# Kernel tuning notes

Measured on AMD Instinct MI355X. Metric: run time of the kernel, lower is better.

Reference implementation:

```python
import jax, jax.numpy as jnp
import numpy as np

B, S, E, H, STEPS = 32, 2048, 300, 256, 24


def setup_inputs() -> dict:
    key = jax.random.key(0)
    ks = jax.random.split(key, 16)
    sc = 0.05
    inp = {
        "input_ids": jax.random.normal(ks[0], (B, S, E), dtype=jnp.float32),
        "tree_ids": jax.random.randint(ks[1], (B, STEPS, S), 0, S),
        "tree_ids_r": jax.random.randint(ks[2], (B, STEPS, S), 0, S),
        "tree_ids_l": jax.random.randint(ks[3], (B, STEPS, S), 0, S),
        # N-ary (binary) TreeLSTM parameters (Tai et al. 2015)
        "W_iou": jax.random.normal(ks[4], (E, 3 * H), dtype=jnp.float32) * sc,
        "b_iou": jnp.zeros((3 * H,), dtype=jnp.float32),
        "U_iou_l": jax.random.normal(ks[5], (H, 3 * H), dtype=jnp.float32) * sc,
        "U_iou_r": jax.random.normal(ks[6], (H, 3 * H), dtype=jnp.float32) * sc,
        "W_f": jax.random.normal(ks[7], (E, H), dtype=jnp.float32) * sc,
        "b_f": jnp.zeros((H,), dtype=jnp.float32),
        "U_f_ll": jax.random.normal(ks[8], (H, H), dtype=jnp.float32) * sc,
        "U_f_lr": jax.random.normal(ks[9], (H, H), dtype=jnp.float32) * sc,
        "U_f_rl": jax.random.normal(ks[10], (H, H), dtype=jnp.float32) * sc,
        "U_f_rr": jax.random.normal(ks[11], (H, H), dtype=jnp.float32) * sc,
    }
    return inp


def _gather_nodes(t, idx):
    # t: [B,S,H], idx: [B,S] -> [B,S,H]
    return jnp.take_along_axis(t, idx[..., None], axis=1)


def reference(input_ids, tree_ids, tree_ids_r, tree_ids_l,
              W_iou, b_iou, U_iou_l, U_iou_r,
              W_f, b_f, U_f_ll, U_f_lr, U_f_rl, U_f_rr):
    dt = input_ids.dtype
    h0 = jnp.zeros((B, S, H), dtype=dt)
    c0 = jnp.zeros((B, S, H), dtype=dt)
    # input projections are step-invariant: compute once
    x_iou = input_ids @ W_iou + b_iou          # [B,S,3H]
    x_f = input_ids @ W_f + b_f                # [B,S,H]
    bidx = jnp.arange(B)[:, None]              # [B,1]

    def step(carry, ids):
        h, c = carry
        idd, idl, idr = ids                    # each [B,S]
        h_l = _gather_nodes(h, idl); c_l = _gather_nodes(c, idl)
        h_r = _gather_nodes(h, idr); c_r = _gather_nodes(c, idr)
        iou = x_iou + h_l @ U_iou_l + h_r @ U_iou_r
        i, o, u = jnp.split(iou, 3, axis=-1)
        i = jax.nn.sigmoid(i); o = jax.nn.sigmoid(o); u = jnp.tanh(u)
        f_l = jax.nn.sigmoid(x_f + h_l @ U_f_ll + h_r @ U_f_lr)
        f_r = jax.nn.sigmoid(x_f + h_l @ U_f_rl + h_r @ U_f_rr)
        c_new = i * u + f_l * c_l + f_r * c_r
        h_new = o * jnp.tanh(c_new)
        # scatter updates to destination node ids; slot 0 is the null slot
        h = h.at[bidx, idd].set(h_new)
        c = c.at[bidx, idd].set(c_new)
        h = h.at[:, 0].set(0.0)
        c = c.at[:, 0].set(0.0)
        return (h, c), None

    ids_seq = (jnp.transpose(tree_ids, (1, 0, 2)),
               jnp.transpose(tree_ids_l, (1, 0, 2)),
               jnp.transpose(tree_ids_r, (1, 0, 2)))
    (h, c), _ = jax.lax.scan(step, (h0, c0), ids_seq)

    roots = tree_ids[:, -1, :].max(axis=1)     # [B]
    h_root = jnp.take_along_axis(
        h, jnp.broadcast_to(roots[:, None, None], (B, 1, H)), axis=1)[:, 0]
    return (h, c, h_root)
```

## Files before the change

kernel.cpp:

```cpp
#include <hip/hip_runtime.h>
#include <hip/hip_bf16.h>
#include <math.h>

#define B_     32
#define S_     2048
#define E_     300
#define H_     256
#define STEPS_ 24
#define BS_    (B_ * S_)
#define NPACK  1280
#define KSL    16
#define KSLP   10
#define COPYB  1024

typedef __bf16 bf16x8 __attribute__((ext_vector_type(8)));
typedef float  f32x4  __attribute__((ext_vector_type(4)));

__device__ __forceinline__ float sigm(float x) {
    return 1.0f / (1.0f + __expf(-x));
}
__device__ __forceinline__ float fast_tanh(float x) {
    return 2.0f * sigm(2.0f * x) - 1.0f;
}

__global__ __launch_bounds__(256) void pack_B_kernel(
    const float* __restrict__ U_iou_l, const float* __restrict__ U_iou_r,
    const float* __restrict__ U_f_ll,  const float* __restrict__ U_f_lr,
    const float* __restrict__ U_f_rl,  const float* __restrict__ U_f_rr,
    __hip_bfloat16* __restrict__ Bp)
{
    const int idx = blockIdx.x * 256 + threadIdx.x;
    if (idx >= KSL * NPACK * 32) return;
    const int ks = idx / (NPACK * 32);
    const int rem = idx - ks * (NPACK * 32);
    const int p = rem >> 5;
    const int kin = rem & 31;
    const int k = ks * 32 + kin;
    const int w = p / 80;
    const int rg = p - w * 80;
    const int g = rg >> 4;
    const int c = w * 16 + (rg & 15);
    float v;
    if (g < 3) {
        const int col = g * 256 + c;
        v = (k < 256) ? U_iou_l[k * 768 + col] : U_iou_r[(k - 256) * 768 + col];
    } else if (g == 3) {
        v = (k < 256) ? U_f_ll[k * 256 + c] : U_f_lr[(k - 256) * 256 + c];
    } else {
        v = (k < 256) ? U_f_rl[k * 256 + c] : U_f_rr[(k - 256) * 256 + c];
    }
    Bp[idx] = __float2bfloat16(v);
}

__global__ __launch_bounds__(256) void pack_W_kernel(
    const float* __restrict__ W_iou, const float* __restrict__ W_f,
    __hip_bfloat16* __restrict__ Wp)
{
    const int idx = blockIdx.x * 256 + threadIdx.x;
    if (idx >= KSLP * 1024 * 32) return;
    const int ks = idx / (1024 * 32);
    const int rem = idx - ks * (1024 * 32);
    const int p = rem >> 5;
    const int kin = rem & 31;
    const int k = ks * 32 + kin;
    const int cw = p >> 6;
    const int g = (p >> 4) & 3;
    const int col = cw * 16 + (p & 15);
    float v = 0.f;
    if (k < E_) v = (g < 3) ? W_iou[k * 768 + g * 256 + col] : W_f[k * 256 + col];
    Wp[idx] = __float2bfloat16(v);
}

__global__ __launch_bounds__(256) void winner_kernel(
    const int* __restrict__ tree_ids, int* __restrict__ winner)
{
    const int idx = blockIdx.x * 256 + threadIdx.x;
    if (idx >= B_ * STEPS_ * S_) return;
    const int b = idx / (STEPS_ * S_);
    const int rem = idx - b * (STEPS_ * S_);
    const int t = rem / S_;
    const int s = rem - t * S_;
    const int d = tree_ids[idx];
    if ((unsigned)d < (unsigned)S_)
        atomicMax(&winner[(size_t)t * BS_ + b * S_ + d], s);
}

__global__ __launch_bounds__(256) void compact_kernel(
    const int* __restrict__ winner, int* __restrict__ compact,
    int* __restrict__ count)
{
    const int tb = blockIdx.x;
    const int tid = threadIdx.x;
    const int* w = winner + (size_t)tb * S_;
    int* cmp = compact + (size_t)tb * S_;
    __shared__ int scan_[256];
    __shared__ int base_;
    if (tid == 0) base_ = 0;
    __syncthreads();
    for (int chunk = 0; chunk < S_ / 256; ++chunk) {
        const int d = chunk * 256 + tid;
        const int s = w[d];
        const int p = (d != 0 && s >= 0) ? 1 : 0;
        int v = p;
        scan_[tid] = v;
        __syncthreads();
        for (int off = 1; off < 256; off <<= 1) {
            const int add = (tid >= off) ? scan_[tid - off] : 0;
            __syncthreads();
            v += add;
            scan_[tid] = v;
            __syncthreads();
        }
        const int mybase = base_;
        if (p) cmp[mybase + v - 1] = (s << 11) | d;
        __syncthreads();
        if (tid == 0) base_ += scan_[255];
        __syncthreads();
    }
    if (tid == 0) count[tb] = base_;
}

__global__ __launch_bounds__(256) void proj_kernel(
    const float* __restrict__ input, const __hip_bfloat16* __restrict__ Wp,
    const float* __restrict__ b_iou, const float* __restrict__ b_f,
    __hip_bfloat16* __restrict__ x_pack)
{
    __shared__ __hip_bfloat16 Ash[16][328];
    const int tid = threadIdx.x;
    const int row0 = blockIdx.x * 16;

    for (int it = 0; it < 5; ++it) {
        const int idx = tid + it * 256;
        const int r = idx / 80;
        const int c4 = idx - r * 80;
        float4 v = make_float4(0.f, 0.f, 0.f, 0.f);
        if (c4 < 75) v = *(const float4*)(input + (size_t)(row0 + r) * E_ + c4 * 4);
        union { __hip_bfloat16 h[4]; uint2 u; } tconv;
        tconv.h[0] = __float2bfloat16(v.x);
        tconv.h[1] = __float2bfloat16(v.y);
        tconv.h[2] = __float2bfloat16(v.z);
        tconv.h[3] = __float2bfloat16(v.w);
        *(uint2*)&Ash[r][c4 * 4] = tconv.u;
    }
    __syncthreads();

    const int lane = tid & 63;
    const int wave = tid >> 6;
    const int m16 = lane & 15;
    const int q = lane >> 4;

    f32x4 acc[16];
    const f32x4 z4 = {0.f, 0.f, 0.f, 0.f};
#pragma unroll
    for (int nt = 0; nt < 16; ++nt) acc[nt] = z4;

    const __hip_bfloat16* wp = Wp + ((size_t)(wave * 256 + m16)) * 32 + q * 8;
    for (int ks = 0; ks < KSLP; ++ks) {
        const bf16x8 a = *reinterpret_cast<const bf16x8*>(&Ash[m16][ks * 32 + q * 8]);
        const __hip_bfloat16* wk = wp + (size_t)ks * 32768;
#pragma unroll
        for (int nt = 0; nt < 16; ++nt) {
            const bf16x8 bb = *reinterpret_cast<const bf16x8*>(wk + nt * 512);
            acc[nt] = __builtin_amdgcn_mfma_f32_16x16x32_bf16(a, bb, acc[nt], 0, 0, 0);
        }
    }

#pragma unroll
    for (int j = 0; j < 4; ++j) {
        const int row = row0 + q * 4 + j;
        const size_t xrow = (size_t)row * 1024;
#pragma unroll
        for (int chunk = 0; chunk < 4; ++chunk) {
            const int c = (wave * 4 + chunk) * 16 + m16;
            union { __hip_bfloat16 h[4]; uint2 u; } pk;
            pk.h[0] = __float2bfloat16(acc[chunk * 4 + 0][j] + b_iou[c]);
            pk.h[1] = __float2bfloat16(acc[chunk * 4 + 1][j] + b_iou[256 + c]);
            pk.h[2] = __float2bfloat16(acc[chunk * 4 + 2][j] + b_iou[512 + c]);
            pk.h[3] = __float2bfloat16(acc[chunk * 4 + 3][j] + b_f[c]);
            *(uint2*)(x_pack + xrow + (size_t)c * 4) = pk.u;
        }
    }
}

__global__ __launch_bounds__(256, 4) void step_kernel(
    const __hip_bfloat16* __restrict__ h_cur, const __hip_bfloat16* __restrict__ c_cur,
    __hip_bfloat16* __restrict__ h_next, __hip_bfloat16* __restrict__ c_next,
    const int* __restrict__ tree_ids_l, const int* __restrict__ tree_ids_r,
    const int* __restrict__ winner_t, const int* __restrict__ compact,
    const int* __restrict__ count, const __hip_bfloat16* __restrict__ x_pack,
    const __hip_bfloat16* __restrict__ Bp, int t)
{
    const int tid = threadIdx.x;

    if (blockIdx.x < COPYB) {
        const uint4* h_cur4 = (const uint4*)h_cur;
        const uint4* c_cur4 = (const uint4*)c_cur;
        uint4* h_next4 = (uint4*)h_next;
        uint4* c_next4 = (uint4*)c_next;
#pragma unroll
        for (int i = 0; i < 8; ++i) {
            const int idx = blockIdx.x * 256 + tid + i * (COPYB * 256);
            const int row = idx >> 5;
            const int d = row & (S_ - 1);
            if (d == 0) {
                const uint4 z = make_uint4(0u, 0u, 0u, 0u);
                h_next4[idx] = z;
                c_next4[idx] = z;
            } else if (winner_t[row] < 0) {
                h_next4[idx] = h_cur4[idx];
                c_next4[idx] = c_cur4[idx];
            }
        }
        return;
    }

    const int sb     = blockIdx.x - COPYB;
    const int grp    = sb >> 5;
    const int l32    = sb & 31;
    const int nq     = l32 >> 3;
    const int tile_g = grp * 8 + (l32 & 7);
    const int b    = tile_g >> 6;
    const int tile = tile_g & 63;
    const int nAct = count[t * B_ + b];
    const int s0 = tile * 32;
    if (s0 >= nAct) return;

    __shared__ __hip_bfloat16 Ash[32][520];
    __shared__ int sS[32], sD[32], sIdl[32], sIdr[32];

    const int* cmp = compact + ((size_t)(t * B_ + b)) * S_;
    if (tid < 32) {
        const int gi = s0 + tid;
        const int pair = (gi < nAct) ? cmp[gi] : 0;
        sS[tid] = pair >> 11;
        sD[tid] = pair & 2047;
    }
    __syncthreads();

    const int* idl_b = tree_ids_l + ((size_t)b * STEPS_ + t) * S_;
    const int* idr_b = tree_ids_r + ((size_t)b * STEPS_ + t) * S_;
    if (tid < 32)       sIdl[tid]      = idl_b[sS[tid]];
    else if (tid < 64)  sIdr[tid - 32] = idr_b[sS[tid - 32]];
    __syncthreads();

#pragma unroll
    for (int it = 0; it < 8; ++it) {
        const int idx = tid + it * 256;
        const int r = idx >> 6;
        const int ch = idx & 63;
        const int half = ch >> 5;
        const int c16 = ch & 31;
        const int src = half ? sIdr[r] : sIdl[r];
        const uint4 v = *(const uint4*)(h_cur + ((size_t)(b * S_) + src) * H_ + c16 * 8);
        *(uint4*)&Ash[r][half * 256 + c16 * 8] = v;
    }
    __syncthreads();

    const int lane = tid & 63;
    const int wave = tid >> 6;
    const int m16 = lane & 15;
    const int q = lane >> 4;
    const int w16 = nq * 4 + wave;
    const int cg = w16 * 16 + m16;

    f32x4 acc[2][5];
#pragma unroll
    for (int sm = 0; sm < 2; ++sm) {
#pragma unroll
        for (int j = 0; j < 4; ++j) {
            const int r = sm * 16 + q * 4 + j;
            float xi = 0.f, xo = 0.f, xu = 0.f, xf = 0.f;
            if (sD[r] != 0) {
                const size_t xrow = ((size_t)(b * S_ + sS[r])) * 1024;
                union { uint2 u; __hip_bfloat16 x[4]; } xv;
                xv.u = *(const uint2*)(x_pack + xrow + (size_t)cg * 4);
                xi = __bfloat162float(xv.x[0]);
                xo = __bfloat162float(xv.x[1]);
                xu = __bfloat162float(xv.x[2]);
                xf = __bfloat162float(xv.x[3]);
            }
            acc[sm][0][j] = xi;
            acc[sm][1][j] = xo;
            acc[sm][2][j] = xu;
            acc[sm][3][j] = xf;
            acc[sm][4][j] = xf;
        }
    }

    const __hip_bfloat16* bp_base =
        Bp + ((size_t)(w16 * 80 + m16)) * 32 + q * 8;

    for (int ks = 0; ks < KSL; ++ks) {
        const bf16x8 a0 = *reinterpret_cast<const bf16x8*>(&Ash[m16][ks * 32 + q * 8]);
        const bf16x8 a1 = *reinterpret_cast<const bf16x8*>(&Ash[16 + m16][ks * 32 + q * 8]);
        const __hip_bfloat16* bk = bp_base + (size_t)ks * (NPACK * 32);
        bf16x8 bfrag[5];
#pragma unroll
        for (int g = 0; g < 5; ++g)
            bfrag[g] = *reinterpret_cast<const bf16x8*>(bk + g * 512);
#pragma unroll
        for (int g = 0; g < 5; ++g) {
            acc[0][g] = __builtin_amdgcn_mfma_f32_16x16x32_bf16(a0, bfrag[g], acc[0][g], 0, 0, 0);
            acc[1][g] = __builtin_amdgcn_mfma_f32_16x16x32_bf16(a1, bfrag[g], acc[1][g], 0, 0, 0);
        }
    }

    const __hip_bfloat16* cb = c_cur + (size_t)(b * S_) * H_ + cg;
#pragma unroll
    for (int sm = 0; sm < 2; ++sm) {
#pragma unroll
        for (int j = 0; j < 4; ++j) {
            const int r = sm * 16 + q * 4 + j;
            const int d = sD[r];
            if (d == 0) continue;
            const size_t orow = ((size_t)(b * S_ + d)) * H_;
            const float ig = sigm(acc[sm][0][j]);
            const float og = sigm(acc[sm][1][j]);
            const float ug = fast_tanh(acc[sm][2][j]);
            const float fl = sigm(acc[sm][3][j]);
            const float fr = sigm(acc[sm][4][j]);
            const float cl = __bfloat162float(cb[(size_t)sIdl[r] * H_]);
            const float cr = __bfloat162float(cb[(size_t)sIdr[r] * H_]);
            const float cn = ig * ug + fl * cl + fr * cr;
            const float hn = og * fast_tanh(cn);
            c_next[orow + cg] = __float2bfloat16(cn);
            h_next[orow + cg] = __float2bfloat16(hn);
        }
    }
}

__global__ __launch_bounds__(256) void convert_kernel(
    const __hip_bfloat16* __restrict__ h, const __hip_bfloat16* __restrict__ c,
    float* __restrict__ out_h, float* __restrict__ out_c)
{
    const size_t i = ((size_t)blockIdx.x * 256 + threadIdx.x) * 8;
#pragma unroll
    for (int j = 0; j < 8; ++j) {
        out_h[i + j] = __bfloat162float(h[i + j]);
        out_c[i + j] = __bfloat162float(c[i + j]);
    }
}

__global__ __launch_bounds__(256) void root_kernel(
    const int* __restrict__ tree_ids,
    const __hip_bfloat16* __restrict__ h, float* __restrict__ h_root)
{
    const int b = blockIdx.x;
    const int tid = threadIdx.x;
    const int* ids = tree_ids + ((size_t)b * STEPS_ + (STEPS_ - 1)) * S_;
    __shared__ int red[256];
    int m = 0;
    for (int s = tid; s < S_; s += 256) m = max(m, ids[s]);
    red[tid] = m;
    __syncthreads();
    for (int off = 128; off > 0; off >>= 1) {
        if (tid < off) red[tid] = max(red[tid], red[tid + off]);
        __syncthreads();
    }
    const int root = red[0];
    h_root[(size_t)b * H_ + tid] =
        __bfloat162float(h[((size_t)(b * S_) + root) * H_ + tid]);
}

extern "C" void kernel_launch(void* const* d_in, const int* in_sizes, int n_in,
                              void* d_out, int out_size, void* d_ws, size_t ws_size,
                              hipStream_t stream)
{
    const float* input_ids  = (const float*)d_in[0];
    const int*   tree_ids   = (const int*)d_in[1];
    const int*   tree_ids_r = (const int*)d_in[2];
    const int*   tree_ids_l = (const int*)d_in[3];
    const float* W_iou   = (const float*)d_in[4];
    const float* b_iou   = (const float*)d_in[5];
    const float* U_iou_l = (const float*)d_in[6];
    const float* U_iou_r = (const float*)d_in[7];
    const float* W_f     = (const float*)d_in[8];
    const float* b_f     = (const float*)d_in[9];
    const float* U_f_ll  = (const float*)d_in[10];
    const float* U_f_lr  = (const float*)d_in[11];
    const float* U_f_rl  = (const float*)d_in[12];
    const float* U_f_rr  = (const float*)d_in[13];

    float* out = (float*)d_out;
    float* out_h = out;
    float* out_c = out + (size_t)BS_ * H_;
    float* out_root = out + (size_t)2 * BS_ * H_;

    char* ws = (char*)d_ws;
    __hip_bfloat16* x_pack = (__hip_bfloat16*)(ws);
    __hip_bfloat16* hA     = (__hip_bfloat16*)(ws + 134217728ull);
    __hip_bfloat16* cA     = (__hip_bfloat16*)(ws + 167772160ull);
    int*            winner = (int*)(ws + 201326592ull);
    __hip_bfloat16* Bp     = (__hip_bfloat16*)(ws + 207618048ull);
    __hip_bfloat16* Wp     = (__hip_bfloat16*)(ws + 208928768ull);
    __hip_bfloat16* hB     = (__hip_bfloat16*)out_h;
    __hip_bfloat16* cB     = (__hip_bfloat16*)out_c;
    int* compact = (int*)((char*)out_h + 33554432ull);
    int* cnt     = compact + (size_t)STEPS_ * B_ * S_;

    hipMemsetAsync(hA, 0, (size_t)BS_ * H_ * sizeof(__hip_bfloat16), stream);
    hipMemsetAsync(cA, 0, (size_t)BS_ * H_ * sizeof(__hip_bfloat16), stream);
    hipMemsetAsync(winner, 0xFF, (size_t)STEPS_ * BS_ * sizeof(int), stream);

    pack_B_kernel<<<(KSL * NPACK * 32 + 255) / 256, 256, 0, stream>>>(
        U_iou_l, U_iou_r, U_f_ll, U_f_lr, U_f_rl, U_f_rr, Bp);
    pack_W_kernel<<<(KSLP * 1024 * 32 + 255) / 256, 256, 0, stream>>>(W_iou, W_f, Wp);
    winner_kernel<<<(B_ * STEPS_ * S_) / 256, 256, 0, stream>>>(tree_ids, winner);
    compact_kernel<<<STEPS_ * B_, 256, 0, stream>>>(winner, compact, cnt);
    proj_kernel<<<BS_ / 16, 256, 0, stream>>>(input_ids, Wp, b_iou, b_f, x_pack);

    for (int t = 0; t < STEPS_; ++t) {
        const __hip_bfloat16* hc = (t & 1) ? hB : hA;
        const __hip_bfloat16* cc = (t & 1) ? cB : cA;
        __hip_bfloat16*       hn = (t & 1) ? hA : hB;
        __hip_bfloat16*       cn = (t & 1) ? cA : cB;
        const int* wt = winner + (size_t)t * BS_;

        step_kernel<<<COPYB + B_ * 64 * 4, 256, 0, stream>>>(
            hc, cc, hn, cn, tree_ids_l, tree_ids_r, wt,
            compact, cnt, x_pack, Bp, t);
    }

    convert_kernel<<<(BS_ * H_ / 8) / 256, 256, 0, stream>>>(hA, cA, out_h, out_c);
    root_kernel<<<B_, 256, 0, stream>>>(tree_ids, hA, out_root);
}
```

Baseline: 4.763 ms.

## Retile input projection GEMM to 64-row blocks split over column quarters

The input projection kernel now stages 64 rows of input per block instead of 16. Each block handles one quarter of the output columns, so each wave computes a 4x4 grid of MFMA tiles and reuses each B fragment across four row tiles. The grid is reordered so that neighbouring blocks share the same rows. This cuts redundant global reads of the packed weights per output element and hoists the bias loads. In exchange, each block reads its input rows four times (once per column quarter), and the larger LDS footprint lowers occupancy.

```diff
diff --git a/kernel.cpp b/kernel.cpp
--- a/kernel.cpp
+++ b/kernel.cpp
@@ -120,16 +120,20 @@
     if (tid == 0) count[tb] = base_;
 }
 
-__global__ __launch_bounds__(256) void proj_kernel(
+__global__ __launch_bounds__(256, 3) void proj_kernel(
     const float* __restrict__ input, const __hip_bfloat16* __restrict__ Wp,
     const float* __restrict__ b_iou, const float* __restrict__ b_f,
     __hip_bfloat16* __restrict__ x_pack)
 {
-    __shared__ __hip_bfloat16 Ash[16][328];
+    __shared__ __hip_bfloat16 Ash[64][328];
     const int tid = threadIdx.x;
-    const int row0 = blockIdx.x * 16;
-
-    for (int it = 0; it < 5; ++it) {
+    const int grp = blockIdx.x >> 5;
+    const int l32 = blockIdx.x & 31;
+    const int cb  = l32 >> 3;
+    const int rg  = grp * 8 + (l32 & 7);
+    const int row0 = rg * 64;
+
+    for (int it = 0; it < 20; ++it) {
         const int idx = tid + it * 256;
         const int r = idx / 80;
         const int c4 = idx - r * 80;
@@ -148,35 +152,48 @@
     const int wave = tid >> 6;
     const int m16 = lane & 15;
     const int q = lane >> 4;
-
-    f32x4 acc[16];
+    const int chunk = cb * 4 + wave;
+    const int c = chunk * 16 + m16;
+
+    f32x4 acc[4][4];
     const f32x4 z4 = {0.f, 0.f, 0.f, 0.f};
 #pragma unroll
-    for (int nt = 0; nt < 16; ++nt) acc[nt] = z4;
-
-    const __hip_bfloat16* wp = Wp + ((size_t)(wave * 256 + m16)) * 32 + q * 8;
+    for (int s = 0; s < 4; ++s)
+#pragma unroll
+        for (int g = 0; g < 4; ++g) acc[s][g] = z4;
+
+    const __hip_bfloat16* wpb = Wp + ((size_t)(chunk * 64 + m16)) * 32 + q * 8;
     for (int ks = 0; ks < KSLP; ++ks) {
-        const bf16x8 a = *reinterpret_cast<const bf16x8*>(&Ash[m16][ks * 32 + q * 8]);
-        const __hip_bfloat16* wk = wp + (size_t)ks * 32768;
-#pragma unroll
-        for (int nt = 0; nt < 16; ++nt) {
-            const bf16x8 bb = *reinterpret_cast<const bf16x8*>(wk + nt * 512);
-            acc[nt] = __builtin_amdgcn_mfma_f32_16x16x32_bf16(a, bb, acc[nt], 0, 0, 0);
-        }
-    }
-
-#pragma unroll
-    for (int j = 0; j < 4; ++j) {
-        const int row = row0 + q * 4 + j;
-        const size_t xrow = (size_t)row * 1024;
-#pragma unroll
-        for (int chunk = 0; chunk < 4; ++chunk) {
-            const int c = (wave * 4 + chunk) * 16 + m16;
+        bf16x8 bfrag[4];
+#pragma unroll
+        for (int g = 0; g < 4; ++g)
+            bfrag[g] = *reinterpret_cast<const bf16x8*>(wpb + (size_t)ks * 32768 + g * 512);
+        bf16x8 a[4];
+#pragma unroll
+        for (int s = 0; s < 4; ++s)
+            a[s] = *reinterpret_cast<const bf16x8*>(&Ash[s * 16 + m16][ks * 32 + q * 8]);
+#pragma unroll
+        for (int s = 0; s < 4; ++s)
+#pragma unroll
+            for (int g = 0; g < 4; ++g)
+                acc[s][g] = __builtin_amdgcn_mfma_f32_16x16x32_bf16(a[s], bfrag[g], acc[s][g], 0, 0, 0);
+    }
+
+    const float bi0 = b_iou[c];
+    const float bi1 = b_iou[256 + c];
+    const float bi2 = b_iou[512 + c];
+    const float bf_ = b_f[c];
+#pragma unroll
+    for (int s = 0; s < 4; ++s) {
+#pragma unroll
+        for (int j = 0; j < 4; ++j) {
+            const int row = row0 + s * 16 + q * 4 + j;
+            const size_t xrow = (size_t)row * 1024;
             union { __hip_bfloat16 h[4]; uint2 u; } pk;
-            pk.h[0] = __float2bfloat16(acc[chunk * 4 + 0][j] + b_iou[c]);
-            pk.h[1] = __float2bfloat16(acc[chunk * 4 + 1][j] + b_iou[256 + c]);
-            pk.h[2] = __float2bfloat16(acc[chunk * 4 + 2][j] + b_iou[512 + c]);
-            pk.h[3] = __float2bfloat16(acc[chunk * 4 + 3][j] + b_f[c]);
+            pk.h[0] = __float2bfloat16(acc[s][0][j] + bi0);
+            pk.h[1] = __float2bfloat16(acc[s][1][j] + bi1);
+            pk.h[2] = __float2bfloat16(acc[s][2][j] + bi2);
+            pk.h[3] = __float2bfloat16(acc[s][3][j] + bf_);
             *(uint2*)(x_pack + xrow + (size_t)c * 4) = pk.u;
         }
     }
@@ -407,7 +424,7 @@
     pack_W_kernel<<<(KSLP * 1024 * 32 + 255) / 256, 256, 0, stream>>>(W_iou, W_f, Wp);
     winner_kernel<<<(B_ * STEPS_ * S_) / 256, 256, 0, stream>>>(tree_ids, winner);
     compact_kernel<<<STEPS_ * B_, 256, 0, stream>>>(winner, compact, cnt);
-    proj_kernel<<<BS_ / 16, 256, 0, stream>>>(input_ids, Wp, b_iou, b_f, x_pack);
+    proj_kernel<<<(BS_ / 64) * 4, 256, 0, stream>>>(input_ids, Wp, b_iou, b_f, x_pack);
 
     for (int t = 0; t < STEPS_; ++t) {
         const __hip_bfloat16* hc = (t & 1) ? hB : hA;
```

Measured after the change: 4.677 ms. Within noise of the previous version (-1.8%).
